# Performance work log

Measured on AMD Instinct MI355X. Metric: run time of the kernel, lower is better.

The kernel has to match this reference:

```python
import jax, jax.numpy as jnp
import numpy as np

MARGIN = 0.5
AP_VALUE = 0.8
AN_VALUE = 0.4
ABS_W = 1.0


def setup_inputs() -> dict:
    key = jax.random.key(0)
    k1, k2 = jax.random.split(key)
    bs, d = 16384, 64
    inputs = jax.random.normal(k1, (bs, d), dtype=jnp.float32)
    target = jax.random.randint(k2, (bs,), 0, 64, dtype=jnp.int64)
    return {"inputs": inputs, "target": target}


def reference(inputs, target):
    # L2-normalize features (normalize_feature=True)
    x = inputs / jnp.linalg.norm(inputs, axis=-1, keepdims=True)

    # cross-entropy on normalized features treated as logits
    logp = jax.nn.log_softmax(x, axis=-1)  # [bs, d]
    loss_ce = -jnp.mean(jnp.take_along_axis(logp, target[:, None], axis=1))

    # cosine-similarity matrix [bs, bs]
    dist = x @ x.T

    is_pos = target[None, :] == target[:, None]
    # hard mining: min similarity among positives, max among negatives (per row)
    dist_ap = jnp.min(jnp.where(is_pos, dist, jnp.inf), axis=1)   # [bs]
    dist_an = jnp.max(jnp.where(is_pos, -jnp.inf, dist), axis=1)  # [bs]

    loss = jnp.mean(jax.nn.relu(MARGIN + dist_ap - dist_an))

    # absolute (angular margin) terms
    abs_ap = jax.nn.relu(AP_VALUE - dist_ap)
    abs_an = jax.nn.relu(dist_an - AN_VALUE)
    loss = (jnp.mean(abs_an) + jnp.mean(abs_ap)) * ABS_W + loss

    return loss + loss_ce
```

## Files before the change

kernel.cpp:

```cpp
#include <hip/hip_runtime.h>


#define N_ROWS 16384
#define N_DIM 64

typedef __attribute__((ext_vector_type(8))) short bf16x8;
typedef __attribute__((ext_vector_type(4))) float f32x4;

__device__ inline unsigned short f2bf(float f) {
  unsigned u = __float_as_uint(f);
  unsigned r = u + 0x7fffu + ((u >> 16) & 1u);
  return (unsigned short)(r >> 16);
}

__device__ inline unsigned enc_key(float f) {
  unsigned u = __float_as_uint(f);
  return (u & 0x80000000u) ? ~u : (u | 0x80000000u);
}
__device__ inline float dec_key(unsigned k) {
  unsigned u = (k & 0x80000000u) ? (k ^ 0x80000000u) : ~k;
  return __uint_as_float(u);
}

__device__ inline void g2lds16(const void* g, void* l) {
  __builtin_amdgcn_global_load_lds(
      (const __attribute__((address_space(1))) void*)g,
      (__attribute__((address_space(3))) void*)l, 16, 0, 0);
}

__global__ void prep_kernel(const float* __restrict__ x, const int* __restrict__ tgt,
                            unsigned short* __restrict__ xb, float* __restrict__ ce_row,
                            unsigned* __restrict__ mp_key, unsigned* __restrict__ mn_key,
                            float* __restrict__ out) {
  const int row  = blockIdx.x * 4 + (threadIdx.x >> 6);
  const int lane = threadIdx.x & 63;
  float v  = x[row * N_DIM + lane];
  float ss = v * v;
#pragma unroll
  for (int s = 1; s < 64; s <<= 1) ss += __shfl_xor(ss, s, 64);
  float xn = v * rsqrtf(ss);
  xb[row * N_DIM + lane] = f2bf(xn);

  float mx = xn;
#pragma unroll
  for (int s = 1; s < 64; s <<= 1) mx = fmaxf(mx, __shfl_xor(mx, s, 64));
  float e  = __expf(xn - mx);
  float se = e;
#pragma unroll
  for (int s = 1; s < 64; s <<= 1) se += __shfl_xor(se, s, 64);
  float lse = mx + __logf(se);
  int   t   = tgt[row];
  float xt  = __shfl(xn, t, 64);
  if (lane == 0) {
    ce_row[row] = lse - xt;
    mp_key[row] = 0xFFFFFFFFu;
    mn_key[row] = 0u;
  }
  if (blockIdx.x == 0 && threadIdx.x == 0) out[0] = 0.f;
}

__global__ __launch_bounds__(256, 8)
void mine_kernel(const unsigned short* __restrict__ xb, const int* __restrict__ tgt,
                 unsigned* __restrict__ mp_key, unsigned* __restrict__ mn_key) {
  __shared__ unsigned short Bt[2][1024];
  __shared__ int tjl[N_ROWS / 16];

  const int lane    = threadIdx.x & 63;
  const int wv      = threadIdx.x >> 6;
  const int iblk    = blockIdx.x >> 4;
  const int jspl    = blockIdx.x & 15;
  const int rowbase = iblk * 128 + wv * 32;
  const int m = lane & 15, q = lane >> 4;
  const int jbase = jspl * (N_ROWS / 16);

  bf16x8 a[2][2];
#pragma unroll
  for (int tr = 0; tr < 2; ++tr) {
    const unsigned short* p = xb + (rowbase + tr * 16 + m) * N_DIM + q * 8;
    a[tr][0] = *(const bf16x8*)(p);
    a[tr][1] = *(const bf16x8*)(p + 32);
  }
  int ti[2][4];
#pragma unroll
  for (int tr = 0; tr < 2; ++tr)
#pragma unroll
    for (int r = 0; r < 4; ++r)
      ti[tr][r] = tgt[rowbase + tr * 16 + q * 4 + r];

  float mp[8], mn[8];
#pragma unroll
  for (int k = 0; k < 8; ++k) { mp[k] = __builtin_inff(); mn[k] = -__builtin_inff(); }

  for (int k = threadIdx.x; k < N_ROWS / 16; k += 256) tjl[k] = tgt[jbase + k];

  const unsigned short* srcbase =
      xb + (jbase + wv * 8 + (lane >> 3)) * N_DIM +
      (((lane & 7) ^ ((lane >> 3) & 7)) * 8);

  if (wv < 2) g2lds16(srcbase, &Bt[0][wv * 512]);
  __syncthreads();

  const int roff0 = m * 128 + ((q * 16) ^ ((m & 7) << 4));
  const int roff1 = m * 128 + (((64) + q * 16) ^ ((m & 7) << 4));

  for (int jc = 0; jc < 64; ++jc) {
    const int p = jc & 1;
    if (wv < 2 && jc < 63)
      g2lds16(srcbase + (jc + 1) * 16 * N_DIM, &Bt[p ^ 1][wv * 512]);

    const char* bb = (const char*)&Bt[p][0];
    const bf16x8 cb0 = *(const bf16x8*)(bb + roff0);
    const bf16x8 cb1 = *(const bf16x8*)(bb + roff1);
    const int    ctj = tjl[jc * 16 + m];

#pragma unroll
    for (int tr = 0; tr < 2; ++tr) {
      f32x4 acc = {0.f, 0.f, 0.f, 0.f};
      acc = __builtin_amdgcn_mfma_f32_16x16x32_bf16(a[tr][0], cb0, acc, 0, 0, 0);
      acc = __builtin_amdgcn_mfma_f32_16x16x32_bf16(a[tr][1], cb1, acc, 0, 0, 0);
#pragma unroll
      for (int r = 0; r < 4; ++r) {
        const bool  pos = (ctj == ti[tr][r]);
        const float d   = acc[r];
        const int   k   = tr * 4 + r;
        mp[k] = fminf(mp[k], pos ? d : __builtin_inff());
        mn[k] = fmaxf(mn[k], pos ? -__builtin_inff() : d);
      }
    }
    __syncthreads();
  }

#pragma unroll
  for (int s = 1; s < 16; s <<= 1) {
#pragma unroll
    for (int k = 0; k < 8; ++k) {
      mp[k] = fminf(mp[k], __shfl_xor(mp[k], s, 64));
      mn[k] = fmaxf(mn[k], __shfl_xor(mn[k], s, 64));
    }
  }
  if (m == 0) {
#pragma unroll
    for (int tr = 0; tr < 2; ++tr)
#pragma unroll
      for (int r = 0; r < 4; ++r) {
        const int row = rowbase + tr * 16 + q * 4 + r;
        atomicMin(&mp_key[row], enc_key(mp[tr * 4 + r]));
        atomicMax(&mn_key[row], enc_key(mn[tr * 4 + r]));
      }
  }
}

__global__ void finalize_kernel(const unsigned* __restrict__ mp_key, const unsigned* __restrict__ mn_key,
                                const float* __restrict__ ce_row, float* __restrict__ out) {
  __shared__ float red[16];
  float s = 0.f;
#pragma unroll
  for (int it = 0; it < 2; ++it) {
    const int r = it * 8192 + blockIdx.x * 1024 + threadIdx.x;
    float ap = dec_key(mp_key[r]);
    float an = dec_key(mn_key[r]);
    s += fmaxf(0.5f + ap - an, 0.f) + fmaxf(0.8f - ap, 0.f) +
         fmaxf(an - 0.4f, 0.f) + ce_row[r];
  }
#pragma unroll
  for (int sh = 1; sh < 64; sh <<= 1) s += __shfl_xor(s, sh, 64);
  const int wv = threadIdx.x >> 6;
  if ((threadIdx.x & 63) == 0) red[wv] = s;
  __syncthreads();
  if (threadIdx.x == 0) {
    float t = 0.f;
#pragma unroll
    for (int w = 0; w < 16; ++w) t += red[w];
    atomicAdd(out, t * (1.0f / N_ROWS));
  }
}

extern "C" void kernel_launch(void* const* d_in, const int* in_sizes, int n_in,
                              void* d_out, int out_size, void* d_ws, size_t ws_size,
                              hipStream_t stream) {
  const float* x   = (const float*)d_in[0];
  const int*   tgt = (const int*)d_in[1];
  char* ws = (char*)d_ws;

  unsigned short* xb     = (unsigned short*)ws;
  unsigned*       mp_key = (unsigned*)(ws + (2u << 20));
  unsigned*       mn_key = (unsigned*)(ws + (2u << 20) + (64u << 10));
  float*          ce_row = (float*)(ws + (2u << 20) + (128u << 10));
  float*          out    = (float*)d_out;

  prep_kernel<<<N_ROWS / 4, 256, 0, stream>>>(x, tgt, xb, ce_row, mp_key, mn_key, out);
  mine_kernel<<<(N_ROWS / 128) * 16, 256, 0, stream>>>(xb, tgt, mp_key, mn_key);
  finalize_kernel<<<8, 1024, 0, stream>>>(mp_key, mn_key, ce_row, out);
}
```

Measured before the change: 159.6 us.

## Stage four column tiles per barrier in mine kernel with all waves loading

The mining loop now loads four 16-row column tiles per phase into a larger double-buffered LDS area, with all four waves issuing global-to-LDS copies, and synchronizes once per phase instead of once per tile. This aims to cut the per-tile barrier and load-issue overhead and give each prefetch more compute to hide behind. Target labels in LDS are stored as 16-bit values to offset the larger B buffer. LDS use per block grows, which may limit occupancy.

```diff
diff --git a/kernel.cpp b/kernel.cpp
--- a/kernel.cpp
+++ b/kernel.cpp
@@ -62,8 +62,8 @@
 __global__ __launch_bounds__(256, 8)
 void mine_kernel(const unsigned short* __restrict__ xb, const int* __restrict__ tgt,
                  unsigned* __restrict__ mp_key, unsigned* __restrict__ mn_key) {
-  __shared__ unsigned short Bt[2][1024];
-  __shared__ int tjl[N_ROWS / 16];
+  __shared__ unsigned short Bt[2][4][1024];
+  __shared__ unsigned short tjl[N_ROWS / 16];
 
   const int lane    = threadIdx.x & 63;
   const int wv      = threadIdx.x >> 6;
@@ -91,40 +91,50 @@
 #pragma unroll
   for (int k = 0; k < 8; ++k) { mp[k] = __builtin_inff(); mn[k] = -__builtin_inff(); }
 
-  for (int k = threadIdx.x; k < N_ROWS / 16; k += 256) tjl[k] = tgt[jbase + k];
-
-  const unsigned short* srcbase =
-      xb + (jbase + wv * 8 + (lane >> 3)) * N_DIM +
-      (((lane & 7) ^ ((lane >> 3) & 7)) * 8);
-
-  if (wv < 2) g2lds16(srcbase, &Bt[0][wv * 512]);
+  for (int k = threadIdx.x; k < N_ROWS / 16; k += 256)
+    tjl[k] = (unsigned short)tgt[jbase + k];
+
+  const unsigned short* src0 =
+      xb + (jbase + (lane >> 3)) * N_DIM + (((lane & 7) ^ ((lane >> 3) & 7)) * 8);
+
+  {
+    const unsigned short* s = src0 + (wv * 16) * N_DIM;
+    g2lds16(s,             (unsigned short*)&Bt[0][wv][0] + lane * 8);
+    g2lds16(s + 8 * N_DIM, (unsigned short*)&Bt[0][wv][0] + 512 + lane * 8);
+  }
   __syncthreads();
 
   const int roff0 = m * 128 + ((q * 16) ^ ((m & 7) << 4));
   const int roff1 = m * 128 + (((64) + q * 16) ^ ((m & 7) << 4));
 
-  for (int jc = 0; jc < 64; ++jc) {
-    const int p = jc & 1;
-    if (wv < 2 && jc < 63)
-      g2lds16(srcbase + (jc + 1) * 16 * N_DIM, &Bt[p ^ 1][wv * 512]);
-
-    const char* bb = (const char*)&Bt[p][0];
-    const bf16x8 cb0 = *(const bf16x8*)(bb + roff0);
-    const bf16x8 cb1 = *(const bf16x8*)(bb + roff1);
-    const int    ctj = tjl[jc * 16 + m];
-
-#pragma unroll
-    for (int tr = 0; tr < 2; ++tr) {
-      f32x4 acc = {0.f, 0.f, 0.f, 0.f};
-      acc = __builtin_amdgcn_mfma_f32_16x16x32_bf16(a[tr][0], cb0, acc, 0, 0, 0);
-      acc = __builtin_amdgcn_mfma_f32_16x16x32_bf16(a[tr][1], cb1, acc, 0, 0, 0);
-#pragma unroll
-      for (int r = 0; r < 4; ++r) {
-        const bool  pos = (ctj == ti[tr][r]);
-        const float d   = acc[r];
-        const int   k   = tr * 4 + r;
-        mp[k] = fminf(mp[k], pos ? d : __builtin_inff());
-        mn[k] = fmaxf(mn[k], pos ? -__builtin_inff() : d);
+  for (int ph = 0; ph < 16; ++ph) {
+    const int pb = ph & 1;
+    if (ph < 15) {
+      const unsigned short* s = src0 + ((ph + 1) * 64 + wv * 16) * N_DIM;
+      g2lds16(s,             (unsigned short*)&Bt[pb ^ 1][wv][0] + lane * 8);
+      g2lds16(s + 8 * N_DIM, (unsigned short*)&Bt[pb ^ 1][wv][0] + 512 + lane * 8);
+    }
+#pragma unroll
+    for (int j4 = 0; j4 < 4; ++j4) {
+      const int jc = ph * 4 + j4;
+      const char* bb = (const char*)&Bt[pb][j4][0];
+      const bf16x8 cb0 = *(const bf16x8*)(bb + roff0);
+      const bf16x8 cb1 = *(const bf16x8*)(bb + roff1);
+      const int    ctj = tjl[jc * 16 + m];
+
+#pragma unroll
+      for (int tr = 0; tr < 2; ++tr) {
+        f32x4 acc = {0.f, 0.f, 0.f, 0.f};
+        acc = __builtin_amdgcn_mfma_f32_16x16x32_bf16(a[tr][0], cb0, acc, 0, 0, 0);
+        acc = __builtin_amdgcn_mfma_f32_16x16x32_bf16(a[tr][1], cb1, acc, 0, 0, 0);
+#pragma unroll
+        for (int r = 0; r < 4; ++r) {
+          const bool  pos = (ctj == ti[tr][r]);
+          const float d   = acc[r];
+          const int   k   = tr * 4 + r;
+          mp[k] = fminf(mp[k], pos ? d : __builtin_inff());
+          mn[k] = fmaxf(mn[k], pos ? -__builtin_inff() : d);
+        }
       }
     }
     __syncthreads();
```

Result: slower. 406.0 us (+154.4%).

## Stream B tiles directly into registers with prefetch instead of LDS double buffer

Applied to the files above, without the earlier changes.

The mining kernel no longer stages each 16-row B tile into a swizzled LDS double buffer with global_load_lds. Each wave now loads its B fragments straight from global memory into registers, prefetching the next tile one iteration ahead. This removes the per-iteration __syncthreads. Row labels are packed into bytes and the column labels are stored as ushort in LDS, which lowers register and LDS use but assumes labels fit in 8 bits. The workspace layout gains a 4 KB gap so the last prefetch, which reads past the end of xb, stays in bounds, at the cost of four waves redundantly loading the same tile through the cache.

```diff
diff --git a/kernel.cpp b/kernel.cpp
--- a/kernel.cpp
+++ b/kernel.cpp
@@ -20,12 +20,6 @@
 __device__ inline float dec_key(unsigned k) {
   unsigned u = (k & 0x80000000u) ? (k ^ 0x80000000u) : ~k;
   return __uint_as_float(u);
-}
-
-__device__ inline void g2lds16(const void* g, void* l) {
-  __builtin_amdgcn_global_load_lds(
-      (const __attribute__((address_space(1))) void*)g,
-      (__attribute__((address_space(3))) void*)l, 16, 0, 0);
 }
 
 __global__ void prep_kernel(const float* __restrict__ x, const int* __restrict__ tgt,
@@ -62,8 +56,7 @@
 __global__ __launch_bounds__(256, 8)
 void mine_kernel(const unsigned short* __restrict__ xb, const int* __restrict__ tgt,
                  unsigned* __restrict__ mp_key, unsigned* __restrict__ mn_key) {
-  __shared__ unsigned short Bt[2][1024];
-  __shared__ int tjl[N_ROWS / 16];
+  __shared__ unsigned short tjl[N_ROWS / 16];
 
   const int lane    = threadIdx.x & 63;
   const int wv      = threadIdx.x >> 6;
@@ -80,38 +73,35 @@
     a[tr][0] = *(const bf16x8*)(p);
     a[tr][1] = *(const bf16x8*)(p + 32);
   }
-  int ti[2][4];
+  unsigned tip[2];
 #pragma unroll
-  for (int tr = 0; tr < 2; ++tr)
+  for (int tr = 0; tr < 2; ++tr) {
+    unsigned vv = 0;
 #pragma unroll
     for (int r = 0; r < 4; ++r)
-      ti[tr][r] = tgt[rowbase + tr * 16 + q * 4 + r];
+      vv |= ((unsigned)tgt[rowbase + tr * 16 + q * 4 + r] & 0xffu) << (8 * r);
+    tip[tr] = vv;
+  }
 
   float mp[8], mn[8];
 #pragma unroll
   for (int k = 0; k < 8; ++k) { mp[k] = __builtin_inff(); mn[k] = -__builtin_inff(); }
 
-  for (int k = threadIdx.x; k < N_ROWS / 16; k += 256) tjl[k] = tgt[jbase + k];
-
-  const unsigned short* srcbase =
-      xb + (jbase + wv * 8 + (lane >> 3)) * N_DIM +
-      (((lane & 7) ^ ((lane >> 3) & 7)) * 8);
-
-  if (wv < 2) g2lds16(srcbase, &Bt[0][wv * 512]);
+  for (int k = threadIdx.x; k < N_ROWS / 16; k += 256)
+    tjl[k] = (unsigned short)tgt[jbase + k];
   __syncthreads();
 
-  const int roff0 = m * 128 + ((q * 16) ^ ((m & 7) << 4));
-  const int roff1 = m * 128 + (((64) + q * 16) ^ ((m & 7) << 4));
+  const unsigned short* pB = xb + (jbase + m) * N_DIM + q * 8;
+  bf16x8 nb0 = *(const bf16x8*)(pB);
+  bf16x8 nb1 = *(const bf16x8*)(pB + 32);
 
+#pragma unroll 1
   for (int jc = 0; jc < 64; ++jc) {
-    const int p = jc & 1;
-    if (wv < 2 && jc < 63)
-      g2lds16(srcbase + (jc + 1) * 16 * N_DIM, &Bt[p ^ 1][wv * 512]);
-
-    const char* bb = (const char*)&Bt[p][0];
-    const bf16x8 cb0 = *(const bf16x8*)(bb + roff0);
-    const bf16x8 cb1 = *(const bf16x8*)(bb + roff1);
-    const int    ctj = tjl[jc * 16 + m];
+    const bf16x8 cb0 = nb0, cb1 = nb1;
+    const unsigned ctj = (unsigned)tjl[jc * 16 + m] & 0xffu;
+    pB += 16 * N_DIM;
+    nb0 = *(const bf16x8*)(pB);
+    nb1 = *(const bf16x8*)(pB + 32);
 
 #pragma unroll
     for (int tr = 0; tr < 2; ++tr) {
@@ -120,14 +110,13 @@
       acc = __builtin_amdgcn_mfma_f32_16x16x32_bf16(a[tr][1], cb1, acc, 0, 0, 0);
 #pragma unroll
       for (int r = 0; r < 4; ++r) {
-        const bool  pos = (ctj == ti[tr][r]);
+        const bool  pos = (((tip[tr] >> (8 * r)) & 0xffu) == ctj);
         const float d   = acc[r];
         const int   k   = tr * 4 + r;
         mp[k] = fminf(mp[k], pos ? d : __builtin_inff());
         mn[k] = fmaxf(mn[k], pos ? -__builtin_inff() : d);
       }
     }
-    __syncthreads();
   }
 
 #pragma unroll
@@ -183,9 +172,9 @@
   char* ws = (char*)d_ws;
 
   unsigned short* xb     = (unsigned short*)ws;
-  unsigned*       mp_key = (unsigned*)(ws + (2u << 20));
-  unsigned*       mn_key = (unsigned*)(ws + (2u << 20) + (64u << 10));
-  float*          ce_row = (float*)(ws + (2u << 20) + (128u << 10));
+  unsigned*       mp_key = (unsigned*)(ws + (2u << 20) + (4u << 10));
+  unsigned*       mn_key = (unsigned*)(ws + (2u << 20) + (4u << 10) + (64u << 10));
+  float*          ce_row = (float*)(ws + (2u << 20) + (4u << 10) + (128u << 10));
   float*          out    = (float*)d_out;
 
   prep_kernel<<<N_ROWS / 4, 256, 0, stream>>>(x, tgt, xb, ce_row, mp_key, mn_key, out);
```

Measured after the change: 185.2 us. +16.1%, slower.
